# Kernel optimization log

Measured on AMD Instinct MI355X. Metric: run time of the kernel, lower is better.

## Reference

```python
import jax, jax.numpy as jnp
import numpy as np

BS, N, C = 512, 18, 2048
EPS = 1e-12
BN_SCALE = 1.0 / np.sqrt(1.0 + 1e-5)  # eval-mode BN with running_mean=0, running_var=1


def _normalize(v):
    # F.normalize(p=2, dim=2, eps=1e-12)
    n = jnp.linalg.norm(v, axis=2, keepdims=True)
    return v / jnp.maximum(n, EPS)


def _bn_relu(v, gamma, beta):
    # BatchNorm2d in eval mode (running_mean=0, running_var=1) followed by ReLU
    return jax.nn.relu(v * (gamma * BN_SCALE) + beta)


def _safe_sqrt(r):
    # forward-identical to sqrt (r >= 0 here); avoids NaN grad at r == 0 (diagonal)
    pos = r > 0
    return jnp.where(pos, jnp.sqrt(jnp.where(pos, r, 1.0)), 0.0)


def setup_inputs() -> dict:
    key = jax.random.key(0)
    ks = jax.random.split(key, 10)
    s = 0.02
    return {
        "x": jax.random.normal(ks[0], (BS, N, C), jnp.float32),
        "part_coordinate": jax.random.uniform(ks[1], (BS, N, 4), jnp.float32),
        # conv1: C -> 3 (1x1)
        "w1": jax.random.normal(ks[2], (3, C), jnp.float32) * s,
        "b1": jnp.zeros((3,), jnp.float32),
        # conv2: 4 -> C, BN, ReLU, C -> 3
        "w2a": jax.random.normal(ks[3], (C, 4), jnp.float32) * s,
        "b2a": jnp.zeros((C,), jnp.float32),
        "g2": jnp.ones((C,), jnp.float32),
        "be2": jnp.zeros((C,), jnp.float32),
        "w2b": jax.random.normal(ks[4], (3, C), jnp.float32) * s,
        "b2b": jnp.zeros((3,), jnp.float32),
        # conv: C -> C, BN, ReLU
        "wc": jax.random.normal(ks[5], (C, C), jnp.float32) * s,
        "bc": jnp.zeros((C,), jnp.float32),
        "gc": jnp.ones((C,), jnp.float32),
        "bec": jnp.zeros((C,), jnp.float32),
        # conv3: C -> C, BN, ReLU
        "w3": jax.random.normal(ks[6], (C, C), jnp.float32) * s,
        "b3": jnp.zeros((C,), jnp.float32),
        "g3": jnp.ones((C,), jnp.float32),
        "be3": jnp.zeros((C,), jnp.float32),
    }


def reference(x, part_coordinate, w1, b1, w2a, b2a, g2, be2, w2b, b2b,
              wc, bc, gc, bec, w3, b3, g3, be3):
    # z1 = softmax(conv1(x)) over the 3 clusters
    z1 = jax.nn.softmax(jnp.einsum('bnc,kc->bnk', x, w1) + b1, axis=2)  # [B,N,3]

    # distance_list1: cosine affinities of x and z1
    xn = _normalize(x)
    d1_1 = jnp.einsum('bnc,bmc->bnm', xn, xn)       # [B,N,N]
    z1n = _normalize(z1)
    d2_1 = jnp.einsum('bnk,bmk->bnm', z1n, z1n)     # [B,N,N]

    # z2 = softmax(conv2(part_coordinate))
    h = _bn_relu(jnp.einsum('bnf,cf->bnc', part_coordinate, w2a) + b2a, g2, be2)
    z2 = jax.nn.softmax(jnp.einsum('bnc,kc->bnk', h, w2b) + b2b, axis=2)  # [B,N,3]

    # distance_list2: spatial-center distance + cosine affinity of z2
    yc = part_coordinate[..., 0] + jnp.floor(part_coordinate[..., 2] / 2)
    xc = part_coordinate[..., 1] + jnp.floor(part_coordinate[..., 3] / 2)
    dy = (yc[:, None, :] - yc[:, :, None]) ** 2
    dx = (xc[:, None, :] - xc[:, :, None]) ** 2
    d1_2 = 1.0 - 2.0 * _safe_sqrt(dx + dy)          # [B,N,N]
    z2n = _normalize(z2)
    d2_2 = jnp.einsum('bnk,bmk->bnm', z2n, z2n)     # [B,N,N]

    # encode / decode aggregation over 3 cluster nodes
    z = z1 + z2                                      # [B,N,3]
    enc = z / (jnp.sum(z, axis=1, keepdims=True) + EPS)
    dec = z / (jnp.sum(z, axis=2, keepdims=True) + EPS)
    u = jnp.einsum('bnk,bnc->bkc', enc, x)           # [B,3,C]
    u = _bn_relu(jnp.einsum('bkc,dc->bkd', u, wc) + bc, gc, bec)
    y = jnp.einsum('bnk,bkc->bnc', dec, u)           # [B,N,C]
    y = _bn_relu(jnp.einsum('bnc,dc->bnd', y, w3) + b3, g3, be3) + x

    return (y, d2_1, d1_1, d2_2, d1_2)
```

## Files before the change

kernel.cpp:

```cpp
#include <hip/hip_runtime.h>

#define BS   512
#define NPTS 18
#define CH   2048
#define EPSF 1e-12f
#define BNS  0.9999950000374997f

typedef unsigned short ushort_t;
typedef __attribute__((ext_vector_type(8)))  short bfrag;
typedef __attribute__((ext_vector_type(4)))  float f32x4v;
typedef __attribute__((ext_vector_type(16))) float f32x16;

__device__ inline ushort_t bf16_rne(float f) {
  union { float f; unsigned int u; } c; c.f = f;
  unsigned int u = c.u;
  u += 0x7fffu + ((u >> 16) & 1u);
  return (ushort_t)(u >> 16);
}
__device__ inline float bf16_to_f(ushort_t s) {
  union { float f; unsigned int u; } c; c.u = ((unsigned int)s) << 16;
  return c.f;
}
__device__ inline bfrag cvt8(float4 a, float4 b) {
  bfrag r;
  r[0]=(short)bf16_rne(a.x); r[1]=(short)bf16_rne(a.y);
  r[2]=(short)bf16_rne(a.z); r[3]=(short)bf16_rne(a.w);
  r[4]=(short)bf16_rne(b.x); r[5]=(short)bf16_rne(b.y);
  r[6]=(short)bf16_rne(b.z); r[7]=(short)bf16_rne(b.w);
  return r;
}

__global__ __launch_bounds__(256) void k_fused(
    const float* __restrict__ x, const float* __restrict__ pc,
    const float* __restrict__ w1,
    const float* __restrict__ w2a, const float* __restrict__ b2a,
    const float* __restrict__ g2, const float* __restrict__ be2,
    const float* __restrict__ w2b,
    const float* __restrict__ wc, const float* __restrict__ w3,
    ushort_t* __restrict__ wc_bf, ushort_t* __restrict__ w3_bf,
    float* __restrict__ Glp, float* __restrict__ l2p)
{
  const int blk = blockIdx.x, tid = threadIdx.x;

  if (blk >= BS*4) {
    const int cb = blk - BS*4;
    const int n4 = CH*CH/4;
    #pragma unroll
    for (int k = 0; k < 4; k++) {
      int gid = (cb*4 + k)*256 + tid;
      const float* src; ushort_t* dst; int i;
      if (gid < n4) { src = wc; dst = wc_bf; i = gid; }
      else          { src = w3; dst = w3_bf; i = gid - n4; }
      float4 v = ((const float4*)src)[i];
      ushort4 o;
      o.x = bf16_rne(v.x); o.y = bf16_rne(v.y);
      o.z = bf16_rne(v.z); o.w = bf16_rne(v.w);
      ((ushort4*)dst)[i] = o;
    }
    return;
  }

  __shared__ __align__(16) float lxf[NPTS*512];
  __shared__ float Gt[4][378];
  const int bq = blk, b = bq >> 2, q = bq & 3;
  const int lane = tid & 63, wv = tid >> 6;

  {
    const int lane16 = lane*16;
    #pragma unroll
    for (int it = 0; it < 9; it++) {
      int ldst = it*4096 + wv*1024 + lane16;
      int row  = ldst >> 11;
      int off  = (ldst & 2047) ^ ((row & 7) << 4);
      const float* gsrc = x + ((size_t)b*NPTS + row)*CH + q*512 + (off >> 2);
      __builtin_amdgcn_global_load_lds(
          (const __attribute__((address_space(1))) void*)gsrc,
          (__attribute__((address_space(3))) void*)((char*)lxf + it*4096 + wv*1024),
          16, 0, 0);
    }
  }

  float zacc[5][3];
  {
    const int p0 = wv*5;
    const int np = (wv == 3) ? 3 : 5;
    float4 pq[5];
    #pragma unroll
    for (int j = 0; j < 5; j++)
      pq[j] = *(const float4*)(pc + (size_t)b*NPTS*4 + (p0 + (j < np ? j : 0))*4);
    #pragma unroll
    for (int j = 0; j < 5; j++) { zacc[j][0]=0.f; zacc[j][1]=0.f; zacc[j][2]=0.f; }
    #pragma unroll 2
    for (int it = 0; it < 8; it++) {
      int c = q*512 + it*64 + lane;
      const float4 wa = *(const float4*)(w2a + (size_t)c*4);
      float bb = b2a[c], gg = g2[c]*BNS, be = be2[c];
      float wb0 = w2b[c], wb1 = w2b[CH+c], wb2 = w2b[2*CH+c];
      #pragma unroll
      for (int j = 0; j < 5; j++) {
        float v = fmaf(pq[j].w, wa.w, fmaf(pq[j].z, wa.z,
                  fmaf(pq[j].y, wa.y, fmaf(pq[j].x, wa.x, bb))));
        float h = fmaxf(fmaf(v, gg, be), 0.f);
        zacc[j][0] = fmaf(h, wb0, zacc[j][0]);
        zacc[j][1] = fmaf(h, wb1, zacc[j][1]);
        zacc[j][2] = fmaf(h, wb2, zacc[j][2]);
      }
    }
    #pragma unroll
    for (int j = 0; j < 5; j++) {
      if (j < np) {
        #pragma unroll
        for (int k = 0; k < 3; k++) {
          float v = zacc[j][k];
          #pragma unroll
          for (int off = 32; off; off >>= 1) v += __shfl_xor(v, off);
          if (lane == 0) l2p[(size_t)bq*54 + (p0+j)*3 + k] = v;
        }
      }
    }
  }

  asm volatile("s_waitcnt vmcnt(0)" ::: "memory");
  __syncthreads();

  {
    const int rc = lane & 31, kh = lane >> 5;
    const int arow = (rc < NPTS) ? rc : (NPTS-1);
    const int amsk = (arow & 7) << 4;
    const int abase = arow*2048;
    const bool isw = (rc >= NPTS) && (rc < NPTS+3);
    const int wrow = isw ? (rc - NPTS) : 0;
    const float* wp = w1 + (size_t)wrow*CH + q*512 + wv*128 + kh*8;
    f32x16 acc0 = {0.f,0.f,0.f,0.f,0.f,0.f,0.f,0.f,0.f,0.f,0.f,0.f,0.f,0.f,0.f,0.f};
    f32x16 acc1 = acc0;
    #pragma unroll
    for (int j = 0; j < 8; j++) {
      const int cb = (wv*128 + j*16 + kh*8)*4;
      float4 a0 = *(const float4*)((const char*)lxf + abase + (cb ^ amsk));
      float4 a1 = *(const float4*)((const char*)lxf + abase + ((cb + 16) ^ amsk));
      bfrag av = cvt8(a0, a1);
      bfrag bv = av;
      if (isw) bv = cvt8(*(const float4*)(wp + j*16), *(const float4*)(wp + j*16 + 4));
      if (j & 1) acc1 = __builtin_amdgcn_mfma_f32_32x32x16_bf16(av, bv, acc1, 0, 0, 0);
      else       acc0 = __builtin_amdgcn_mfma_f32_32x32x16_bf16(av, bv, acc0, 0, 0, 0);
    }
    #pragma unroll
    for (int r = 0; r < 16; r++) {
      int orow = (r & 3) + 8*(r >> 2) + 4*kh;
      if (orow < NPTS && rc < 21) Gt[wv][orow*21 + rc] = acc0[r] + acc1[r];
    }
  }

  __syncthreads();
  for (int t = tid; t < 378; t += 256) {
    float* g = Glp + (size_t)bq*378;
    g[t] = (Gt[0][t] + Gt[1][t]) + (Gt[2][t] + Gt[3][t]);
  }
}

__global__ __launch_bounds__(512) void k_final(
    const float* __restrict__ x, const float* __restrict__ pc,
    const float* __restrict__ b1, const float* __restrict__ b2b,
    const float* __restrict__ Glp, const float* __restrict__ l2p,
    float* __restrict__ d21, float* __restrict__ d11,
    float* __restrict__ d22, float* __restrict__ d12,
    ushort_t* __restrict__ u_pre, float* __restrict__ dec_out)
{
  __shared__ float sGl[378];
  __shared__ float l2s[54];
  __shared__ float z1s[54], z2s[54], encs[54];
  __shared__ float ycs[NPTS], xcs[NPTS];
  __shared__ float n1inv[NPTS], n2inv[NPTS], rinv[NPTS], colinv[3];
  const int b = blockIdx.x, tid = threadIdx.x;

  if (tid < 378) {
    const float* g = Glp + (size_t)b*4*378 + tid;
    sGl[tid] = (g[0] + g[378]) + (g[756] + g[1134]);
  } else if (tid < 432) {
    int t = tid - 378;
    const float* g = l2p + (size_t)b*4*54 + t;
    l2s[t] = (g[0] + g[54]) + (g[108] + g[162]) + b2b[t%3];
  } else if (tid < 450) {
    int n = tid - 432;
    const float* p = pc + (size_t)b*NPTS*4 + n*4;
    ycs[n] = p[0] + floorf(p[2]*0.5f);
    xcs[n] = p[1] + floorf(p[3]*0.5f);
  }
  __syncthreads();

  if (tid < NPTS) {
    int n = tid;
    float a0 = sGl[n*21+18] + b1[0], a1 = sGl[n*21+19] + b1[1], a2 = sGl[n*21+20] + b1[2];
    float mx = fmaxf(a0, fmaxf(a1, a2));
    float e0 = expf(a0-mx), e1 = expf(a1-mx), e2 = expf(a2-mx);
    float inv = 1.f/(e0+e1+e2);
    float z10 = e0*inv, z11 = e1*inv, z12 = e2*inv;
    z1s[n*3+0]=z10; z1s[n*3+1]=z11; z1s[n*3+2]=z12;
    n1inv[n] = 1.f/fmaxf(sqrtf(z10*z10+z11*z11+z12*z12), EPSF);

    float c0 = l2s[n*3+0], c1 = l2s[n*3+1], c2 = l2s[n*3+2];
    mx = fmaxf(c0, fmaxf(c1, c2));
    e0 = expf(c0-mx); e1 = expf(c1-mx); e2 = expf(c2-mx);
    inv = 1.f/(e0+e1+e2);
    float z20 = e0*inv, z21 = e1*inv, z22 = e2*inv;
    z2s[n*3+0]=z20; z2s[n*3+1]=z21; z2s[n*3+2]=z22;
    n2inv[n] = 1.f/fmaxf(sqrtf(z20*z20+z21*z21+z22*z22), EPSF);

    float zr0 = z10+z20, zr1 = z11+z21, zr2 = z12+z22;
    float rinvv = 1.f/((zr0+zr1+zr2) + EPSF);
    dec_out[(size_t)b*54 + n*3 + 0] = zr0*rinvv;
    dec_out[(size_t)b*54 + n*3 + 1] = zr1*rinvv;
    dec_out[(size_t)b*54 + n*3 + 2] = zr2*rinvv;

    rinv[n] = 1.f/fmaxf(sqrtf(sGl[n*21+n]), EPSF);
  }
  __syncthreads();

  if (tid < 3) {
    float s = 0.f;
    #pragma unroll
    for (int n = 0; n < NPTS; n++) s += z1s[n*3+tid] + z2s[n*3+tid];
    colinv[tid] = 1.f/(s + EPSF);
  }
  if (tid < NPTS*NPTS) {
    int t = tid;
    int n = t/NPTS, mm = t - n*NPTS;
    float dd21 = (z1s[n*3]*z1s[mm*3] + z1s[n*3+1]*z1s[mm*3+1] + z1s[n*3+2]*z1s[mm*3+2])
                 * n1inv[n]*n1inv[mm];
    float dd22 = (z2s[n*3]*z2s[mm*3] + z2s[n*3+1]*z2s[mm*3+1] + z2s[n*3+2]*z2s[mm*3+2])
                 * n2inv[n]*n2inv[mm];
    float dd11 = sGl[n*21+mm] * rinv[n]*rinv[mm];
    float dyv = ycs[mm]-ycs[n], dxv = xcs[mm]-xcs[n];
    float r = dxv*dxv + dyv*dyv;
    float dd12 = 1.f - 2.f*((r > 0.f) ? sqrtf(r) : 0.f);
    size_t o = (size_t)b*NPTS*NPTS + t;
    d21[o] = dd21; d11[o] = dd11; d22[o] = dd22; d12[o] = dd12;
  }
  __syncthreads();
  if (tid < 54) encs[tid] = (z1s[tid]+z2s[tid])*colinv[tid%3];
  __syncthreads();

  {
    const int c0 = tid*4;
    const float* xb = x + (size_t)b*NPTS*CH + c0;
    float av0[4], av1[4], av2[4];
    #pragma unroll
    for (int j = 0; j < 4; j++) { av0[j]=0.f; av1[j]=0.f; av2[j]=0.f; }
    #pragma unroll 2
    for (int n = 0; n < NPTS; n++) {
      float4 xv = *(const float4*)(xb + (size_t)n*CH);
      float e0 = encs[n*3+0], e1 = encs[n*3+1], e2 = encs[n*3+2];
      av0[0]=fmaf(e0,xv.x,av0[0]); av0[1]=fmaf(e0,xv.y,av0[1]);
      av0[2]=fmaf(e0,xv.z,av0[2]); av0[3]=fmaf(e0,xv.w,av0[3]);
      av1[0]=fmaf(e1,xv.x,av1[0]); av1[1]=fmaf(e1,xv.y,av1[1]);
      av1[2]=fmaf(e1,xv.z,av1[2]); av1[3]=fmaf(e1,xv.w,av1[3]);
      av2[0]=fmaf(e2,xv.x,av2[0]); av2[1]=fmaf(e2,xv.y,av2[1]);
      av2[2]=fmaf(e2,xv.z,av2[2]); av2[3]=fmaf(e2,xv.w,av2[3]);
    }
    ushort4 o0, o1, o2;
    o0.x=bf16_rne(av0[0]); o0.y=bf16_rne(av0[1]); o0.z=bf16_rne(av0[2]); o0.w=bf16_rne(av0[3]);
    o1.x=bf16_rne(av1[0]); o1.y=bf16_rne(av1[1]); o1.z=bf16_rne(av1[2]); o1.w=bf16_rne(av1[3]);
    o2.x=bf16_rne(av2[0]); o2.y=bf16_rne(av2[1]); o2.z=bf16_rne(av2[2]); o2.w=bf16_rne(av2[3]);
    *(ushort4*)(u_pre + ((size_t)b*3 + 0)*CH + c0) = o0;
    *(ushort4*)(u_pre + ((size_t)b*3 + 1)*CH + c0) = o1;
    *(ushort4*)(u_pre + ((size_t)b*3 + 2)*CH + c0) = o2;
  }
}

#define GM 1536
#define GK 2048
#define GN 2048

#define STAGE(buf, k0) { \
    _Pragma("unroll") \
    for (int i = 0; i < 4; i++) \
      __builtin_amdgcn_global_load_lds( \
          (const __attribute__((address_space(1))) void*)(Ag + (size_t)(i*32 + ldrow)*GK + (k0)), \
          (__attribute__((address_space(3))) void*)(&Asm[buf][i*2048 + wv*512]), 16, 0, 0); \
    _Pragma("unroll") \
    for (int i = 0; i < 2; i++) \
      __builtin_amdgcn_global_load_lds( \
          (const __attribute__((address_space(1))) void*)(Bg + (size_t)(i*32 + ldrow)*GK + (k0)), \
          (__attribute__((address_space(3))) void*)(&Bsm[buf][i*2048 + wv*512]), 16, 0, 0); }

template<int MODE>
__global__ __launch_bounds__(256) void gemm_mfma(
    const ushort_t* __restrict__ A, const ushort_t* __restrict__ B,
    void* __restrict__ Cout, const float* __restrict__ bias,
    const float* __restrict__ gamma, const float* __restrict__ beta)
{
  __shared__ ushort_t Asm[2][128*64];
  __shared__ ushort_t Bsm[2][64*64];
  const int tid  = threadIdx.x;
  const int lane = tid & 63, wv = tid >> 6;
  const int mb = blockIdx.x % (GM/128), nb = blockIdx.x / (GM/128);
  const int wr = (wv >> 1) * 64, wc = (wv & 1) * 32;

  f32x4v acc[4][2];
  #pragma unroll
  for (int m = 0; m < 4; m++)
    #pragma unroll
    for (int n = 0; n < 2; n++)
      acc[m][n] = (f32x4v){0.f, 0.f, 0.f, 0.f};

  const int ldrow = tid >> 3;
  const int ldcol = (((tid & 7) ^ (ldrow & 7)) * 8);
  const ushort_t* Ag = A + (size_t)(mb*128)*GK + ldcol;
  const ushort_t* Bg = B + (size_t)(nb*64)*GK + ldcol;
  const int r15 = lane & 15, khi = lane >> 4;

  STAGE(0, 0)
  __syncthreads();
  for (int t = 0; t < GK/64; ++t) {
    const int cur = t & 1;
    if (t < GK/64 - 1) STAGE(cur ^ 1, (t+1)*64)
    #pragma unroll
    for (int ks = 0; ks < 2; ks++) {
      bfrag af[4], bfv[2];
      #pragma unroll
      for (int m = 0; m < 4; m++) {
        const int ar = wr + m*16 + r15;
        af[m] = *(const bfrag*)(&Asm[cur][ar*64 + ((ks*32 + khi*8) ^ ((ar & 7)*8))]);
      }
      #pragma unroll
      for (int n = 0; n < 2; n++) {
        const int br = wc + n*16 + r15;
        bfv[n] = *(const bfrag*)(&Bsm[cur][br*64 + ((ks*32 + khi*8) ^ ((br & 7)*8))]);
      }
      #pragma unroll
      for (int m = 0; m < 4; m++)
        #pragma unroll
        for (int n = 0; n < 2; n++)
          acc[m][n] = __builtin_amdgcn_mfma_f32_16x16x32_bf16(
              af[m], bfv[n], acc[m][n], 0, 0, 0);
    }
    __syncthreads();
  }

  #pragma unroll
  for (int n = 0; n < 2; n++) {
    const int gc = nb*64 + wc + n*16 + r15;
    float bi = 0.f, ga = 0.f, be = 0.f;
    if (MODE == 1) { bi = bias[gc]; ga = gamma[gc]*BNS; be = beta[gc]; }
    #pragma unroll
    for (int m = 0; m < 4; m++) {
      const int gr0 = mb*128 + wr + m*16 + khi*4;
      #pragma unroll
      for (int r = 0; r < 4; r++) {
        float v = acc[m][n][r];
        if (MODE == 1) {
          v = fmaxf(fmaf(v + bi, ga, be), 0.f);
          ((ushort_t*)Cout)[(size_t)(gr0 + r)*GN + gc] = bf16_rne(v);
        } else {
          ((float*)Cout)[(size_t)(gr0 + r)*GN + gc] = v;
        }
      }
    }
  }
}

__global__ __launch_bounds__(256) void k_epi(
    const float* __restrict__ x, const float* __restrict__ V,
    const float* __restrict__ dec, const float* __restrict__ b3,
    const float* __restrict__ g3, const float* __restrict__ be3,
    float* __restrict__ y)
{
  __shared__ float4 lv[3*512];
  __shared__ float4 lmul[512], ladd[512];
  __shared__ float ld[54];
  const int b = blockIdx.x, tid = threadIdx.x;

  const float4* v4 = (const float4*)(V + (size_t)b*3*CH);
  for (int i = tid; i < 1536; i += 256) lv[i] = v4[i];
  const float4* g34  = (const float4*)g3;
  const float4* b34  = (const float4*)b3;
  const float4* be34 = (const float4*)be3;
  for (int i = tid; i < 512; i += 256) {
    float4 g = g34[i], bb = b34[i], be = be34[i];
    float4 mu, ad;
    mu.x = g.x*BNS; mu.y = g.y*BNS; mu.z = g.z*BNS; mu.w = g.w*BNS;
    ad.x = fmaf(bb.x, mu.x, be.x); ad.y = fmaf(bb.y, mu.y, be.y);
    ad.z = fmaf(bb.z, mu.z, be.z); ad.w = fmaf(bb.w, mu.w, be.w);
    lmul[i] = mu; ladd[i] = ad;
  }
  if (tid < 54) ld[tid] = dec[(size_t)b*54 + tid];
  __syncthreads();

  for (int r = 0; r < NPTS; r++) {
    float d0 = ld[r*3+0], d1 = ld[r*3+1], d2 = ld[r*3+2];
    const float4* xr = (const float4*)(x + ((size_t)b*NPTS + r)*CH);
    float4* yr = (float4*)(y + ((size_t)b*NPTS + r)*CH);
    for (int i = tid; i < 512; i += 256) {
      float4 v0 = lv[i], v1 = lv[512+i], v2 = lv[1024+i];
      float4 mu = lmul[i], ad = ladd[i], xa = xr[i];
      float4 o;
      o.x = fmaxf(fmaf(fmaf(d0,v0.x, fmaf(d1,v1.x, d2*v2.x)), mu.x, ad.x), 0.f) + xa.x;
      o.y = fmaxf(fmaf(fmaf(d0,v0.y, fmaf(d1,v1.y, d2*v2.y)), mu.y, ad.y), 0.f) + xa.y;
      o.z = fmaxf(fmaf(fmaf(d0,v0.z, fmaf(d1,v1.z, d2*v2.z)), mu.z, ad.z), 0.f) + xa.z;
      o.w = fmaxf(fmaf(fmaf(d0,v0.w, fmaf(d1,v1.w, d2*v2.w)), mu.w, ad.w), 0.f) + xa.w;
      yr[i] = o;
    }
  }
}

extern "C" void kernel_launch(void* const* d_in, const int* in_sizes, int n_in,
                              void* d_out, int out_size, void* d_ws, size_t ws_size,
                              hipStream_t stream) {
  const float* x   = (const float*)d_in[0];
  const float* pc  = (const float*)d_in[1];
  const float* w1  = (const float*)d_in[2];
  const float* b1  = (const float*)d_in[3];
  const float* w2a = (const float*)d_in[4];
  const float* b2a = (const float*)d_in[5];
  const float* g2  = (const float*)d_in[6];
  const float* be2 = (const float*)d_in[7];
  const float* w2b = (const float*)d_in[8];
  const float* b2b = (const float*)d_in[9];
  const float* wc  = (const float*)d_in[10];
  const float* bc  = (const float*)d_in[11];
  const float* gc  = (const float*)d_in[12];
  const float* bec = (const float*)d_in[13];
  const float* w3  = (const float*)d_in[14];
  const float* b3  = (const float*)d_in[15];
  const float* g3  = (const float*)d_in[16];
  const float* be3 = (const float*)d_in[17];

  float* out = (float*)d_out;
  float* y   = out;
  float* d21 = out + (size_t)BS*NPTS*CH;
  float* d11 = d21 + (size_t)BS*NPTS*NPTS;
  float* d22 = d11 + (size_t)BS*NPTS*NPTS;
  float* d12 = d22 + (size_t)BS*NPTS*NPTS;

  char* ybytes = (char*)y;
  ushort_t* u_pre_bf = (ushort_t*)(ybytes + 0);
  ushort_t* u_bf     = (ushort_t*)(ybytes + 6291456);
  ushort_t* wc_bf    = (ushort_t*)(ybytes + 12582912);
  ushort_t* w3_bf    = (ushort_t*)(ybytes + 20971520);
  float*    Glp      = (float*)   (ybytes + 29360128);
  float*    l2p      = (float*)   (ybytes + 32456704);

  float* V    = (float*)d_ws;
  float* decb = V + (size_t)BS*3*CH;

  k_fused<<<BS*4 + 2048, 256, 0, stream>>>(x, pc, w1, w2a, b2a, g2, be2, w2b,
                                           wc, w3, wc_bf, w3_bf, Glp, l2p);
  k_final<<<BS, 512, 0, stream>>>(x, pc, b1, b2b, Glp, l2p,
                                  d21, d11, d22, d12, u_pre_bf, decb);
  gemm_mfma<1><<<(GM/128)*(GN/64), 256, 0, stream>>>(u_pre_bf, wc_bf, u_bf, bc, gc, bec);
  gemm_mfma<0><<<(GM/128)*(GN/64), 256, 0, stream>>>(u_bf, w3_bf, V, nullptr, nullptr, nullptr);
  k_epi<<<BS, 256, 0, stream>>>(x, V, decb, b3, g3, be3, y);
}
```

Before: 158.2 us.

## Fuse second GEMM with output epilogue and convert w3 to bf16 on the fly

Replaces the second GEMM and the separate epilogue kernel with one kernel. It loads fp32 w3 directly, packs it to bf16 in registers with v_cvt_pk_bf16_f32, stages V tiles in LDS, and applies the decode/BN/ReLU/residual epilogue in place. This removes the separate w3 bf16 conversion pass, the fp32 V round trip through global memory, and one kernel launch. It also adds an XCD-aware block index remap to both GEMMs. In exchange, the fused GEMM has no double buffering, and the epilogue now reads V rounded to bf16 instead of fp32.

After: 243.4 us. 53.8% more time.

```diff
diff --git a/kernel.cpp b/kernel.cpp
--- a/kernel.cpp
+++ b/kernel.cpp
@@ -29,6 +29,11 @@
   r[6]=(short)bf16_rne(b.z); r[7]=(short)bf16_rne(b.w);
   return r;
 }
+__device__ inline unsigned cvtpk(float lo, float hi) {
+  unsigned r;
+  asm("v_cvt_pk_bf16_f32 %0, %1, %2" : "=v"(r) : "v"(lo), "v"(hi));
+  return r;
+}
 
 __global__ __launch_bounds__(256) void k_fused(
     const float* __restrict__ x, const float* __restrict__ pc,
@@ -36,26 +41,21 @@
     const float* __restrict__ w2a, const float* __restrict__ b2a,
     const float* __restrict__ g2, const float* __restrict__ be2,
     const float* __restrict__ w2b,
-    const float* __restrict__ wc, const float* __restrict__ w3,
-    ushort_t* __restrict__ wc_bf, ushort_t* __restrict__ w3_bf,
+    const float* __restrict__ wc, ushort_t* __restrict__ wc_bf,
     float* __restrict__ Glp, float* __restrict__ l2p)
 {
   const int blk = blockIdx.x, tid = threadIdx.x;
 
   if (blk >= BS*4) {
     const int cb = blk - BS*4;
-    const int n4 = CH*CH/4;
     #pragma unroll
     for (int k = 0; k < 4; k++) {
-      int gid = (cb*4 + k)*256 + tid;
-      const float* src; ushort_t* dst; int i;
-      if (gid < n4) { src = wc; dst = wc_bf; i = gid; }
-      else          { src = w3; dst = w3_bf; i = gid - n4; }
-      float4 v = ((const float4*)src)[i];
+      int i = (cb*4 + k)*256 + tid;
+      float4 v = ((const float4*)wc)[i];
       ushort4 o;
       o.x = bf16_rne(v.x); o.y = bf16_rne(v.y);
       o.z = bf16_rne(v.z); o.w = bf16_rne(v.w);
-      ((ushort4*)dst)[i] = o;
+      ((ushort4*)wc_bf)[i] = o;
     }
     return;
   }
@@ -80,7 +80,6 @@
     }
   }
 
-  float zacc[5][3];
   {
     const int p0 = wv*5;
     const int np = (wv == 3) ? 3 : 5;
@@ -88,6 +87,7 @@
     #pragma unroll
     for (int j = 0; j < 5; j++)
       pq[j] = *(const float4*)(pc + (size_t)b*NPTS*4 + (p0 + (j < np ? j : 0))*4);
+    float zacc[5][3];
     #pragma unroll
     for (int j = 0; j < 5; j++) { zacc[j][0]=0.f; zacc[j][1]=0.f; zacc[j][2]=0.f; }
     #pragma unroll 2
@@ -283,17 +283,17 @@
           (const __attribute__((address_space(1))) void*)(Bg + (size_t)(i*32 + ldrow)*GK + (k0)), \
           (__attribute__((address_space(3))) void*)(&Bsm[buf][i*2048 + wv*512]), 16, 0, 0); }
 
-template<int MODE>
-__global__ __launch_bounds__(256) void gemm_mfma(
+__global__ __launch_bounds__(256) void gemm1(
     const ushort_t* __restrict__ A, const ushort_t* __restrict__ B,
-    void* __restrict__ Cout, const float* __restrict__ bias,
+    ushort_t* __restrict__ Cout, const float* __restrict__ bias,
     const float* __restrict__ gamma, const float* __restrict__ beta)
 {
   __shared__ ushort_t Asm[2][128*64];
   __shared__ ushort_t Bsm[2][64*64];
   const int tid  = threadIdx.x;
   const int lane = tid & 63, wv = tid >> 6;
-  const int mb = blockIdx.x % (GM/128), nb = blockIdx.x / (GM/128);
+  const int wg = (blockIdx.x & 7)*48 + (blockIdx.x >> 3);
+  const int mb = wg % (GM/128), nb = wg / (GM/128);
   const int wr = (wv >> 1) * 64, wc = (wv & 1) * 32;
 
   f32x4v acc[4][2];
@@ -340,65 +340,151 @@
   #pragma unroll
   for (int n = 0; n < 2; n++) {
     const int gc = nb*64 + wc + n*16 + r15;
-    float bi = 0.f, ga = 0.f, be = 0.f;
-    if (MODE == 1) { bi = bias[gc]; ga = gamma[gc]*BNS; be = beta[gc]; }
+    float bi = bias[gc], ga = gamma[gc]*BNS, be = beta[gc];
     #pragma unroll
     for (int m = 0; m < 4; m++) {
       const int gr0 = mb*128 + wr + m*16 + khi*4;
       #pragma unroll
       for (int r = 0; r < 4; r++) {
-        float v = acc[m][n][r];
-        if (MODE == 1) {
-          v = fmaxf(fmaf(v + bi, ga, be), 0.f);
-          ((ushort_t*)Cout)[(size_t)(gr0 + r)*GN + gc] = bf16_rne(v);
-        } else {
-          ((float*)Cout)[(size_t)(gr0 + r)*GN + gc] = v;
+        float v = fmaxf(fmaf(acc[m][n][r] + bi, ga, be), 0.f);
+        Cout[(size_t)(gr0 + r)*GN + gc] = bf16_rne(v);
+      }
+    }
+  }
+}
+
+__global__ __launch_bounds__(256) void gemm_epi(
+    const ushort_t* __restrict__ A, const float* __restrict__ Bw,
+    const float* __restrict__ x, const float* __restrict__ dec,
+    const float* __restrict__ b3, const float* __restrict__ g3,
+    const float* __restrict__ be3, float* __restrict__ y)
+{
+  __shared__ ushort_t Asm[96*64];
+  __shared__ ushort_t Bsm[128*64];
+  __shared__ ushort_t Vl[96*132];
+  __shared__ float decl[32*54];
+  __shared__ float mul_[128], add_[128];
+  const int tid = threadIdx.x, lane = tid & 63, wv = tid >> 6;
+  const int wg = (blockIdx.x & 7)*32 + (blockIdx.x >> 3);
+  const int mb = wg & 15, nb = wg >> 4;
+  const int wr = (wv >> 1)*48, wc = (wv & 1)*64;
+  const int r15 = lane & 15, khi = lane >> 4;
+
+  for (int i = tid; i < 32*54; i += 256) decl[i] = dec[(size_t)mb*1728 + i];
+  if (tid < 128) {
+    float mu = g3[nb*128 + tid]*BNS;
+    mul_[tid] = mu;
+    add_[tid] = fmaf(b3[nb*128 + tid], mu, be3[nb*128 + tid]);
+  }
+
+  f32x4v acc[3][4];
+  #pragma unroll
+  for (int m = 0; m < 3; m++)
+    #pragma unroll
+    for (int n = 0; n < 4; n++)
+      acc[m][n] = (f32x4v){0.f, 0.f, 0.f, 0.f};
+
+  const int brow = tid >> 1, bkh = tid & 1;
+  const float* bsrc = Bw + (size_t)(nb*128 + brow)*2048 + bkh*32;
+  const int bmask = (brow & 7) << 4;
+
+  for (int t = 0; t < 32; ++t) {
+    const int k0 = t*64;
+    float4 bf[8];
+    #pragma unroll
+    for (int j = 0; j < 8; j++) bf[j] = *(const float4*)(bsrc + k0 + j*4);
+    __syncthreads();
+    #pragma unroll
+    for (int i = 0; i < 3; i++) {
+      int u = i*256 + tid;
+      int row = u >> 3, c8 = u & 7;
+      const ushort_t* ga = A + (size_t)(mb*96 + row)*2048 + k0 + ((c8 ^ (row & 7))*8);
+      __builtin_amdgcn_global_load_lds(
+          (const __attribute__((address_space(1))) void*)ga,
+          (__attribute__((address_space(3))) void*)(Asm + (size_t)u*8), 16, 0, 0);
+    }
+    #pragma unroll
+    for (int i = 0; i < 4; i++) {
+      uint4 w;
+      w.x = cvtpk(bf[2*i].x,   bf[2*i].y);
+      w.y = cvtpk(bf[2*i].z,   bf[2*i].w);
+      w.z = cvtpk(bf[2*i+1].x, bf[2*i+1].y);
+      w.w = cvtpk(bf[2*i+1].z, bf[2*i+1].w);
+      int byte = brow*128 + (((bkh*4 + i)*16) ^ bmask);
+      *(uint4*)((char*)Bsm + byte) = w;
+    }
+    asm volatile("s_waitcnt vmcnt(0)" ::: "memory");
+    __syncthreads();
+    #pragma unroll
+    for (int ks = 0; ks < 2; ks++) {
+      bfrag af[3], bfv[4];
+      #pragma unroll
+      for (int m = 0; m < 3; m++) {
+        const int ar = wr + m*16 + r15;
+        af[m] = *(const bfrag*)((const char*)Asm + ar*128 + ((ks*64 + khi*16) ^ ((ar & 7)*16)));
+      }
+      #pragma unroll
+      for (int n = 0; n < 4; n++) {
+        const int br = wc + n*16 + r15;
+        bfv[n] = *(const bfrag*)((const char*)Bsm + br*128 + ((ks*64 + khi*16) ^ ((br & 7)*16)));
+      }
+      #pragma unroll
+      for (int m = 0; m < 3; m++)
+        #pragma unroll
+        for (int n = 0; n < 4; n++)
+          acc[m][n] = __builtin_amdgcn_mfma_f32_16x16x32_bf16(
+              af[m], bfv[n], acc[m][n], 0, 0, 0);
+    }
+  }
+
+  __syncthreads();
+  #pragma unroll
+  for (int n = 0; n < 4; n++) {
+    const int gcl = wc + n*16 + r15;
+    #pragma unroll
+    for (int m = 0; m < 3; m++) {
+      const int gr = wr + m*16 + khi*4;
+      #pragma unroll
+      for (int r = 0; r < 4; r++)
+        Vl[(gr + r)*132 + gcl] = bf16_rne(acc[m][n][r]);
+    }
+  }
+  __syncthreads();
+
+  {
+    const int bb = tid >> 3, cg = tid & 7;
+    float vr[3][16], mu[16], ad[16];
+    #pragma unroll
+    for (int k = 0; k < 3; k++)
+      #pragma unroll
+      for (int cc = 0; cc < 4; cc++) {
+        ushort4 vv = *(const ushort4*)(&Vl[(bb*3 + k)*132 + cg*16 + cc*4]);
+        vr[k][cc*4+0] = bf16_to_f(vv.x); vr[k][cc*4+1] = bf16_to_f(vv.y);
+        vr[k][cc*4+2] = bf16_to_f(vv.z); vr[k][cc*4+3] = bf16_to_f(vv.w);
+      }
+    #pragma unroll
+    for (int j = 0; j < 16; j++) { mu[j] = mul_[cg*16+j]; ad[j] = add_[cg*16+j]; }
+
+    const size_t rowbase = ((size_t)(mb*32 + bb)*NPTS)*CH + nb*128 + cg*16;
+    for (int n = 0; n < NPTS; n++) {
+      float d0 = decl[bb*54 + n*3 + 0];
+      float d1 = decl[bb*54 + n*3 + 1];
+      float d2 = decl[bb*54 + n*3 + 2];
+      const float* xr = x + rowbase + (size_t)n*CH;
+      float* yr = y + rowbase + (size_t)n*CH;
+      #pragma unroll
+      for (int cc = 0; cc < 4; cc++) {
+        float4 xv = *(const float4*)(xr + cc*4);
+        float4 o;
+        #pragma unroll
+        for (int j = 0; j < 4; j++) {
+          int c = cc*4 + j;
+          float val = fmaf(d0, vr[0][c], fmaf(d1, vr[1][c], d2*vr[2][c]));
+          float res = fmaxf(fmaf(val, mu[c], ad[c]), 0.f);
+          ((float*)&o)[j] = res + ((const float*)&xv)[j];
         }
-      }
-    }
-  }
-}
-
-__global__ __launch_bounds__(256) void k_epi(
-    const float* __restrict__ x, const float* __restrict__ V,
-    const float* __restrict__ dec, const float* __restrict__ b3,
-    const float* __restrict__ g3, const float* __restrict__ be3,
-    float* __restrict__ y)
-{
-  __shared__ float4 lv[3*512];
-  __shared__ float4 lmul[512], ladd[512];
-  __shared__ float ld[54];
-  const int b = blockIdx.x, tid = threadIdx.x;
-
-  const float4* v4 = (const float4*)(V + (size_t)b*3*CH);
-  for (int i = tid; i < 1536; i += 256) lv[i] = v4[i];
-  const float4* g34  = (const float4*)g3;
-  const float4* b34  = (const float4*)b3;
-  const float4* be34 = (const float4*)be3;
-  for (int i = tid; i < 512; i += 256) {
-    float4 g = g34[i], bb = b34[i], be = be34[i];
-    float4 mu, ad;
-    mu.x = g.x*BNS; mu.y = g.y*BNS; mu.z = g.z*BNS; mu.w = g.w*BNS;
-    ad.x = fmaf(bb.x, mu.x, be.x); ad.y = fmaf(bb.y, mu.y, be.y);
-    ad.z = fmaf(bb.z, mu.z, be.z); ad.w = fmaf(bb.w, mu.w, be.w);
-    lmul[i] = mu; ladd[i] = ad;
-  }
-  if (tid < 54) ld[tid] = dec[(size_t)b*54 + tid];
-  __syncthreads();
-
-  for (int r = 0; r < NPTS; r++) {
-    float d0 = ld[r*3+0], d1 = ld[r*3+1], d2 = ld[r*3+2];
-    const float4* xr = (const float4*)(x + ((size_t)b*NPTS + r)*CH);
-    float4* yr = (float4*)(y + ((size_t)b*NPTS + r)*CH);
-    for (int i = tid; i < 512; i += 256) {
-      float4 v0 = lv[i], v1 = lv[512+i], v2 = lv[1024+i];
-      float4 mu = lmul[i], ad = ladd[i], xa = xr[i];
-      float4 o;
-      o.x = fmaxf(fmaf(fmaf(d0,v0.x, fmaf(d1,v1.x, d2*v2.x)), mu.x, ad.x), 0.f) + xa.x;
-      o.y = fmaxf(fmaf(fmaf(d0,v0.y, fmaf(d1,v1.y, d2*v2.y)), mu.y, ad.y), 0.f) + xa.y;
-      o.z = fmaxf(fmaf(fmaf(d0,v0.z, fmaf(d1,v1.z, d2*v2.z)), mu.z, ad.z), 0.f) + xa.z;
-      o.w = fmaxf(fmaf(fmaf(d0,v0.w, fmaf(d1,v1.w, d2*v2.w)), mu.w, ad.w), 0.f) + xa.w;
-      yr[i] = o;
+        *(float4*)(yr + cc*4) = o;
+      }
     }
   }
 }
@@ -434,20 +520,17 @@
 
   char* ybytes = (char*)y;
   ushort_t* u_pre_bf = (ushort_t*)(ybytes + 0);
-  ushort_t* u_bf     = (ushort_t*)(ybytes + 6291456);
-  ushort_t* wc_bf    = (ushort_t*)(ybytes + 12582912);
-  ushort_t* w3_bf    = (ushort_t*)(ybytes + 20971520);
-  float*    Glp      = (float*)   (ybytes + 29360128);
-  float*    l2p      = (float*)   (ybytes + 32456704);
-
-  float* V    = (float*)d_ws;
-  float* decb = V + (size_t)BS*3*CH;
-
-  k_fused<<<BS*4 + 2048, 256, 0, stream>>>(x, pc, w1, w2a, b2a, g2, be2, w2b,
-                                           wc, w3, wc_bf, w3_bf, Glp, l2p);
+  ushort_t* wc_bf    = (ushort_t*)(ybytes + 6291456);
+  float*    Glp      = (float*)   (ybytes + 14680064);
+  float*    l2p      = (float*)   (ybytes + 17825792);
+
+  ushort_t* u_bf = (ushort_t*)d_ws;
+  float*    decb = (float*)((char*)d_ws + 6291456);
+
+  k_fused<<<BS*4 + 1024, 256, 0, stream>>>(x, pc, w1, w2a, b2a, g2, be2, w2b,
+                                           wc, wc_bf, Glp, l2p);
   k_final<<<BS, 512, 0, stream>>>(x, pc, b1, b2b, Glp, l2p,
                                   d21, d11, d22, d12, u_pre_bf, decb);
-  gemm_mfma<1><<<(GM/128)*(GN/64), 256, 0, stream>>>(u_pre_bf, wc_bf, u_bf, bc, gc, bec);
-  gemm_mfma<0><<<(GM/128)*(GN/64), 256, 0, stream>>>(u_bf, w3_bf, V, nullptr, nullptr, nullptr);
-  k_epi<<<BS, 256, 0, stream>>>(x, V, decb, b3, g3, be3, y);
-}
+  gemm1<<<(GM/128)*(GN/64), 256, 0, stream>>>(u_pre_bf, wc_bf, u_bf, bc, gc, bec);
+  gemm_epi<<<16*16, 256, 0, stream>>>(u_bf, w3, x, decb, b3, g3, be3, y);
+}
```

## Process whole batch per block in k_fused with double-buffered LDS channel chunks

Applied to the files above, without the earlier changes.

k_fused now assigns one block per batch instead of four blocks per batch (one per 512-channel quarter). Each block loops over the four channel chunks and double-buffers the global-to-LDS loads of x so the next chunk's load overlaps the current chunk's MLP and MFMA work. Partial Gram and z2 sums now stay in registers, so the cross-block partial reduction in k_final disappears. The trade-off is four times fewer compute blocks (512 plus the conversion blocks), doubled LDS per block (lower occupancy), and more serialized work per block.

After: 161.0 us. About the same (+1.7%).

```diff
diff --git a/kernel.cpp b/kernel.cpp
--- a/kernel.cpp
+++ b/kernel.cpp
@@ -42,8 +42,8 @@
 {
   const int blk = blockIdx.x, tid = threadIdx.x;
 
-  if (blk >= BS*4) {
-    const int cb = blk - BS*4;
+  if (blk >= BS) {
+    const int cb = blk - BS;
     const int n4 = CH*CH/4;
     #pragma unroll
     for (int k = 0; k < 4; k++) {
@@ -60,39 +60,54 @@
     return;
   }
 
-  __shared__ __align__(16) float lxf[NPTS*512];
+  __shared__ __align__(16) float lxf[2][NPTS*512];
   __shared__ float Gt[4][378];
-  const int bq = blk, b = bq >> 2, q = bq & 3;
+  const int b = blk;
   const int lane = tid & 63, wv = tid >> 6;
 
-  {
-    const int lane16 = lane*16;
-    #pragma unroll
-    for (int it = 0; it < 9; it++) {
-      int ldst = it*4096 + wv*1024 + lane16;
-      int row  = ldst >> 11;
-      int off  = (ldst & 2047) ^ ((row & 7) << 4);
-      const float* gsrc = x + ((size_t)b*NPTS + row)*CH + q*512 + (off >> 2);
-      __builtin_amdgcn_global_load_lds(
-          (const __attribute__((address_space(1))) void*)gsrc,
-          (__attribute__((address_space(3))) void*)((char*)lxf + it*4096 + wv*1024),
-          16, 0, 0);
-    }
-  }
-
+  const int rc = lane & 31, kh = lane >> 5;
+  const int arow = (rc < NPTS) ? rc : (NPTS-1);
+  const int amsk = (arow & 7) << 4;
+  const int abase = arow*2048;
+  const bool isw = (rc >= NPTS) && (rc < NPTS+3);
+  const int wrow = isw ? (rc - NPTS) : 0;
+
+  const int p0 = wv*5;
+  const int np = (wv == 3) ? 3 : 5;
+  float4 pq[5];
+  #pragma unroll
+  for (int j = 0; j < 5; j++)
+    pq[j] = *(const float4*)(pc + (size_t)b*NPTS*4 + (p0 + (j < np ? j : 0))*4);
+
+  f32x16 acc0 = {0.f,0.f,0.f,0.f,0.f,0.f,0.f,0.f,0.f,0.f,0.f,0.f,0.f,0.f,0.f,0.f};
+  f32x16 acc1 = acc0;
   float zacc[5][3];
-  {
-    const int p0 = wv*5;
-    const int np = (wv == 3) ? 3 : 5;
-    float4 pq[5];
-    #pragma unroll
-    for (int j = 0; j < 5; j++)
-      pq[j] = *(const float4*)(pc + (size_t)b*NPTS*4 + (p0 + (j < np ? j : 0))*4);
-    #pragma unroll
-    for (int j = 0; j < 5; j++) { zacc[j][0]=0.f; zacc[j][1]=0.f; zacc[j][2]=0.f; }
+  #pragma unroll
+  for (int j = 0; j < 5; j++) { zacc[j][0]=0.f; zacc[j][1]=0.f; zacc[j][2]=0.f; }
+
+  const int lane16 = lane*16;
+#define KSTAGE(buf, qq) { \
+    _Pragma("unroll") \
+    for (int it = 0; it < 9; it++) { \
+      int ldst = it*4096 + wv*1024 + lane16; \
+      int row  = ldst >> 11; \
+      int off  = (ldst & 2047) ^ ((row & 7) << 4); \
+      const float* gsrc = x + ((size_t)b*NPTS + row)*CH + (qq)*512 + (off >> 2); \
+      __builtin_amdgcn_global_load_lds( \
+          (const __attribute__((address_space(1))) void*)gsrc, \
+          (__attribute__((address_space(3))) void*)((char*)lxf + (buf)*36864 + it*4096 + wv*1024), \
+          16, 0, 0); \
+    } }
+
+  KSTAGE(0, 0)
+
+  for (int u = 0; u < 4; ++u) {
+    const int cur = u & 1;
+    if (u < 3) KSTAGE(cur ^ 1, u + 1)
+
     #pragma unroll 2
     for (int it = 0; it < 8; it++) {
-      int c = q*512 + it*64 + lane;
+      int c = u*512 + it*64 + lane;
       const float4 wa = *(const float4*)(w2a + (size_t)c*4);
       float bb = b2a[c], gg = g2[c]*BNS, be = be2[c];
       float wb0 = w2b[c], wb1 = w2b[CH+c], wb2 = w2b[2*CH+c];
@@ -106,55 +121,51 @@
         zacc[j][2] = fmaf(h, wb2, zacc[j][2]);
       }
     }
-    #pragma unroll
-    for (int j = 0; j < 5; j++) {
-      if (j < np) {
+
+    if (u < 3) { asm volatile("s_waitcnt vmcnt(9)" ::: "memory"); }
+    else       { asm volatile("s_waitcnt vmcnt(0)" ::: "memory"); }
+    __builtin_amdgcn_sched_barrier(0);
+    __syncthreads();
+
+    {
+      const float* wp = w1 + (size_t)wrow*CH + u*512 + wv*128 + kh*8;
+      const char* lbase = (const char*)lxf + cur*36864 + abase;
+      #pragma unroll
+      for (int j = 0; j < 8; j++) {
+        const int cb2 = (wv*128 + j*16 + kh*8)*4;
+        float4 a0 = *(const float4*)(lbase + (cb2 ^ amsk));
+        float4 a1 = *(const float4*)(lbase + ((cb2 + 16) ^ amsk));
+        bfrag av = cvt8(a0, a1);
+        bfrag bv = av;
+        if (isw) bv = cvt8(*(const float4*)(wp + j*16), *(const float4*)(wp + j*16 + 4));
+        if (j & 1) acc1 = __builtin_amdgcn_mfma_f32_32x32x16_bf16(av, bv, acc1, 0, 0, 0);
+        else       acc0 = __builtin_amdgcn_mfma_f32_32x32x16_bf16(av, bv, acc0, 0, 0, 0);
+      }
+    }
+    __syncthreads();
+  }
+
+  #pragma unroll
+  for (int j = 0; j < 5; j++) {
+    if (j < np) {
+      #pragma unroll
+      for (int k = 0; k < 3; k++) {
+        float v = zacc[j][k];
         #pragma unroll
-        for (int k = 0; k < 3; k++) {
-          float v = zacc[j][k];
-          #pragma unroll
-          for (int off = 32; off; off >>= 1) v += __shfl_xor(v, off);
-          if (lane == 0) l2p[(size_t)bq*54 + (p0+j)*3 + k] = v;
-        }
-      }
-    }
-  }
-
-  asm volatile("s_waitcnt vmcnt(0)" ::: "memory");
-  __syncthreads();
-
-  {
-    const int rc = lane & 31, kh = lane >> 5;
-    const int arow = (rc < NPTS) ? rc : (NPTS-1);
-    const int amsk = (arow & 7) << 4;
-    const int abase = arow*2048;
-    const bool isw = (rc >= NPTS) && (rc < NPTS+3);
-    const int wrow = isw ? (rc - NPTS) : 0;
-    const float* wp = w1 + (size_t)wrow*CH + q*512 + wv*128 + kh*8;
-    f32x16 acc0 = {0.f,0.f,0.f,0.f,0.f,0.f,0.f,0.f,0.f,0.f,0.f,0.f,0.f,0.f,0.f,0.f};
-    f32x16 acc1 = acc0;
-    #pragma unroll
-    for (int j = 0; j < 8; j++) {
-      const int cb = (wv*128 + j*16 + kh*8)*4;
-      float4 a0 = *(const float4*)((const char*)lxf + abase + (cb ^ amsk));
-      float4 a1 = *(const float4*)((const char*)lxf + abase + ((cb + 16) ^ amsk));
-      bfrag av = cvt8(a0, a1);
-      bfrag bv = av;
-      if (isw) bv = cvt8(*(const float4*)(wp + j*16), *(const float4*)(wp + j*16 + 4));
-      if (j & 1) acc1 = __builtin_amdgcn_mfma_f32_32x32x16_bf16(av, bv, acc1, 0, 0, 0);
-      else       acc0 = __builtin_amdgcn_mfma_f32_32x32x16_bf16(av, bv, acc0, 0, 0, 0);
-    }
-    #pragma unroll
-    for (int r = 0; r < 16; r++) {
-      int orow = (r & 3) + 8*(r >> 2) + 4*kh;
-      if (orow < NPTS && rc < 21) Gt[wv][orow*21 + rc] = acc0[r] + acc1[r];
-    }
-  }
-
+        for (int off = 32; off; off >>= 1) v += __shfl_xor(v, off);
+        if (lane == 0) l2p[(size_t)b*54 + (p0+j)*3 + k] = v;
+      }
+    }
+  }
+
+  #pragma unroll
+  for (int r = 0; r < 16; r++) {
+    int orow = (r & 3) + 8*(r >> 2) + 4*kh;
+    if (orow < NPTS && rc < 21) Gt[wv][orow*21 + rc] = acc0[r] + acc1[r];
+  }
   __syncthreads();
   for (int t = tid; t < 378; t += 256) {
-    float* g = Glp + (size_t)bq*378;
-    g[t] = (Gt[0][t] + Gt[1][t]) + (Gt[2][t] + Gt[3][t]);
+    Glp[(size_t)b*378 + t] = (Gt[0][t] + Gt[1][t]) + (Gt[2][t] + Gt[3][t]);
   }
 }
 
@@ -174,12 +185,10 @@
   const int b = blockIdx.x, tid = threadIdx.x;
 
   if (tid < 378) {
-    const float* g = Glp + (size_t)b*4*378 + tid;
-    sGl[tid] = (g[0] + g[378]) + (g[756] + g[1134]);
+    sGl[tid] = Glp[(size_t)b*378 + tid];
   } else if (tid < 432) {
     int t = tid - 378;
-    const float* g = l2p + (size_t)b*4*54 + t;
-    l2s[t] = (g[0] + g[54]) + (g[108] + g[162]) + b2b[t%3];
+    l2s[t] = l2p[(size_t)b*54 + t] + b2b[t%3];
   } else if (tid < 450) {
     int n = tid - 432;
     const float* p = pc + (size_t)b*NPTS*4 + n*4;
@@ -438,13 +447,13 @@
   ushort_t* wc_bf    = (ushort_t*)(ybytes + 12582912);
   ushort_t* w3_bf    = (ushort_t*)(ybytes + 20971520);
   float*    Glp      = (float*)   (ybytes + 29360128);
-  float*    l2p      = (float*)   (ybytes + 32456704);
+  float*    l2p      = (float*)   (ybytes + 30408704);
 
   float* V    = (float*)d_ws;
   float* decb = V + (size_t)BS*3*CH;
 
-  k_fused<<<BS*4 + 2048, 256, 0, stream>>>(x, pc, w1, w2a, b2a, g2, be2, w2b,
-                                           wc, w3, wc_bf, w3_bf, Glp, l2p);
+  k_fused<<<BS + 2048, 256, 0, stream>>>(x, pc, w1, w2a, b2a, g2, be2, w2b,
+                                         wc, w3, wc_bf, w3_bf, Glp, l2p);
   k_final<<<BS, 512, 0, stream>>>(x, pc, b1, b2b, Glp, l2p,
                                   d21, d11, d22, d12, u_pre_bf, decb);
   gemm_mfma<1><<<(GM/128)*(GN/64), 256, 0, stream>>>(u_pre_bf, wc_bf, u_bf, bc, gc, bec);
```
